# Optimization experiments

Measured on AMD Instinct MI355X. Metric: run time of the kernel, lower is better.

## Reference

```python
import jax, jax.numpy as jnp
import numpy as np

N_NODES = 100000


def gcn_conv(x, src, dst, deg_inv_sqrt, W, b):
    # x: [N, Fin], src/dst: [E_total] (self-loops included), W: [Fin, Fout]
    h = x @ W                                  # [N, Fout]
    norm = deg_inv_sqrt[src] * deg_inv_sqrt[dst]  # [E_total]
    msgs = h[src] * norm[:, None]              # [E_total, Fout] gather
    out = jax.ops.segment_sum(msgs, dst, num_segments=N_NODES)  # scatter-add
    return out + b


def setup_inputs() -> dict:
    key = jax.random.key(0)
    k1, k2, k3, k4, k5, k6, k7, k8 = jax.random.split(key, 8)
    input_dim, hidden_dim, out_dim = 4, 64, 2
    n_edges = 3200000
    x = jax.random.normal(k1, (N_NODES, input_dim), dtype=jnp.float32)
    edge_index = jax.random.randint(k2, (2, n_edges), 0, N_NODES, dtype=jnp.int64)
    s1 = 1.0 / np.sqrt(input_dim)
    s2 = 1.0 / np.sqrt(hidden_dim)
    W1 = jax.random.uniform(k3, (input_dim, hidden_dim), jnp.float32, -s1, s1)
    b1 = jnp.zeros((hidden_dim,), jnp.float32)
    W2 = jax.random.uniform(k4, (hidden_dim, hidden_dim), jnp.float32, -s2, s2)
    b2 = jnp.zeros((hidden_dim,), jnp.float32)
    Wf = jax.random.uniform(k5, (hidden_dim, out_dim), jnp.float32, -s2, s2)
    bf = jax.random.uniform(k6, (out_dim,), jnp.float32, -s2, s2)
    return {"x": x, "edge_index": edge_index, "W1": W1, "b1": b1,
            "W2": W2, "b2": b2, "Wf": Wf, "bf": bf}


def reference(x, edge_index, W1, b1, W2, b2, Wf, bf):
    # Add self-loops (PyG GCNConv default)
    loop = jnp.arange(N_NODES, dtype=edge_index.dtype)
    src = jnp.concatenate([edge_index[0], loop])
    dst = jnp.concatenate([edge_index[1], loop])
    # Symmetric normalization: degree on destination after self-loops
    deg = jax.ops.segment_sum(jnp.ones_like(dst, dtype=x.dtype), dst,
                              num_segments=N_NODES)
    deg_inv_sqrt = jnp.where(deg > 0, jax.lax.rsqrt(deg), 0.0)
    h = jax.nn.relu(gcn_conv(x, src, dst, deg_inv_sqrt, W1, b1))
    h = jax.nn.relu(gcn_conv(h, src, dst, deg_inv_sqrt, W2, b2))
    return h @ Wf + bf
```

## Files before the change

### kernel.cpp

```cpp
#include <hip/hip_runtime.h>
#include <hip/hip_bf16.h>

#define N_NODES 100000
#define N_EDGES 3200000
#define NB ((N_NODES + 255) / 256)
#define NBUCKET NB
#define EPB 8192
#define NPB ((N_EDGES + EPB - 1) / EPB)
#define BCAP 11264
#define KF_BLOCKS 1280
#define KF_WAVES (KF_BLOCKS * 4)

__device__ inline unsigned f2bf(float f) {
  unsigned x = __float_as_uint(f);
  return (x + 0x7FFFu + ((x >> 16) & 1u)) >> 16;
}


__global__ void __launch_bounds__(256) k_pass1(const int* __restrict__ src,
                                               const int* __restrict__ dst,
                                               int* __restrict__ gcur,
                                               unsigned int* __restrict__ eb) {
  __shared__ int hist[NBUCKET];
  __shared__ int gbase[NBUCKET];
  int tid = threadIdx.x;
  int base = blockIdx.x * EPB;
  int cnt = min(EPB, N_EDGES - base);
  int n4 = cnt >> 2;
  for (int i = tid; i < NBUCKET; i += 256) hist[i] = 0;
  __syncthreads();
  const int4* d4 = (const int4*)(dst + base);
  const int4* s4 = (const int4*)(src + base);
  unsigned mv[32];
  unsigned short mb[32];
#pragma unroll
  for (int k = 0; k < 8; ++k) {
    int i = tid + (k << 8);
    if (i < n4) {
      int4 dv = d4[i];
      int4 sv = s4[i];
      int b0 = dv.x >> 8, b1_ = dv.y >> 8, b2 = dv.z >> 8, b3 = dv.w >> 8;
      unsigned p0 = atomicAdd(&hist[b0], 1);
      unsigned p1 = atomicAdd(&hist[b1_], 1);
      unsigned p2 = atomicAdd(&hist[b2], 1);
      unsigned p3 = atomicAdd(&hist[b3], 1);
      mv[4 * k + 0] = (unsigned)sv.x | ((unsigned)(dv.x & 255) << 17) | (p0 << 25);
      mv[4 * k + 1] = (unsigned)sv.y | ((unsigned)(dv.y & 255) << 17) | (p1 << 25);
      mv[4 * k + 2] = (unsigned)sv.z | ((unsigned)(dv.z & 255) << 17) | (p2 << 25);
      mv[4 * k + 3] = (unsigned)sv.w | ((unsigned)(dv.w & 255) << 17) | (p3 << 25);
      mb[4 * k + 0] = (unsigned short)b0;
      mb[4 * k + 1] = (unsigned short)b1_;
      mb[4 * k + 2] = (unsigned short)b2;
      mb[4 * k + 3] = (unsigned short)b3;
    } else {
      mb[4 * k + 0] = 0xFFFF; mb[4 * k + 1] = 0xFFFF;
      mb[4 * k + 2] = 0xFFFF; mb[4 * k + 3] = 0xFFFF;
    }
  }
  __syncthreads();
  for (int b = tid; b < NBUCKET; b += 256) {
    int h = hist[b];
    gbase[b] = h ? atomicAdd(&gcur[b], h) : 0;
  }
  __syncthreads();
#pragma unroll
  for (int k = 0; k < 32; ++k) {
    if (mb[k] != 0xFFFF) {
      int b = mb[k];
      unsigned v = mv[k];
      unsigned pos = (unsigned)gbase[b] + (v >> 25);
      if (pos < BCAP) eb[(size_t)b * BCAP + pos] = v & 0x01FFFFFFu;
    }
  }
}


__global__ void __launch_bounds__(256) k_part2(unsigned int* __restrict__ eb,
                                               const int* __restrict__ gcur,
                                               int* __restrict__ rs, int* __restrict__ re,
                                               float* __restrict__ dis,
                                               const float4* __restrict__ x4,
                                               float4* __restrict__ xd) {
  __shared__ int hist[256], scn[256], cur[256];
  __shared__ int tot;
  __shared__ unsigned int stage[BCAP];
  int b = blockIdx.x, tid = threadIdx.x;
  int n0 = b << 8;
  int cnt = gcur[b];
  int base = b * BCAP;
  hist[tid] = 0; cur[tid] = 0;
  __syncthreads();
  for (int i = tid; i < cnt; i += 256)
    atomicAdd(&hist[eb[base + i] >> 17], 1);
  __syncthreads();
  int n = n0 + tid;
  int deg = hist[tid];
  int slots = (n < N_NODES) ? ((deg + 1 + 7) & ~7) : 0;
  int x = slots;
  scn[tid] = x;
  __syncthreads();
  for (int off = 1; off < 256; off <<= 1) {
    int t = (tid >= off) ? scn[tid - off] : 0;
    __syncthreads();
    x += t; scn[tid] = x;
    __syncthreads();
  }
  int excl = x - slots;
  if (tid == 255) tot = x;
  if (n < N_NODES) {
    rs[n]  = base + excl;
    re[n]  = base + excl + deg + 1;
    float dn = rsqrtf((float)(deg + 1));
    dis[n] = dn;
    float4 xv = x4[n];
    float4 w; w.x = xv.x * dn; w.y = xv.y * dn; w.z = xv.z * dn; w.w = xv.w * dn;
    xd[n] = w;
    stage[excl] = (unsigned)n;
    for (int i = deg + 1; i < slots; ++i)
      stage[excl + i] = (unsigned)N_NODES;
  }
  if (b == 0 && tid == 0) xd[N_NODES] = make_float4(0.f, 0.f, 0.f, 0.f);
  scn[tid] = excl + 1;
  __syncthreads();
  for (int i = tid; i < cnt; i += 256) {
    unsigned v = eb[base + i];
    unsigned low = v >> 17;
    int lpos = scn[low] + atomicAdd(&cur[low], 1);
    stage[lpos] = v & 0x1FFFFu;
  }
  __syncthreads();
  int total = tot;
  for (int i = tid; i < total; i += 256)
    eb[base + i] = stage[i];
  if (tid < 16) {
    int gp = total + tid;
    if (gp < BCAP) eb[base + gp] = (unsigned)N_NODES;
  }
}


__global__ void __launch_bounds__(256) k_l1(const float4* __restrict__ xd,
                                            const float* __restrict__ dis,
                                            const int* __restrict__ rs,
                                            const int* __restrict__ re,
                                            const int* __restrict__ csr,
                                            const float* __restrict__ W1,
                                            const float* __restrict__ b1,
                                            unsigned int* __restrict__ h1o) {
  int gt = blockIdx.x * 256 + threadIdx.x;
  int nid = gt >> 2, p = gt & 3;
  if (nid > N_NODES) return;
  if (nid == N_NODES) {
    uint4 z = make_uint4(0u, 0u, 0u, 0u);
    uint4* op = (uint4*)(h1o + nid * 32 + p * 8);
    op[0] = z; op[1] = z;
    return;
  }
  int e0 = rs[nid];
  int it4 = ((re[nid] - e0 + 7) & ~7) >> 2;
  const int* cp = csr + e0 + p;
  float ax = 0.f, ay = 0.f, az = 0.f, aw = 0.f;
#pragma unroll 4
  for (int t = 0; t < it4; ++t) {
    int s = cp[t << 2];
    float4 v = xd[s];
    ax += v.x; ay += v.y; az += v.z; aw += v.w;
  }
  ax += __shfl_xor(ax, 1); ax += __shfl_xor(ax, 2);
  ay += __shfl_xor(ay, 1); ay += __shfl_xor(ay, 2);
  az += __shfl_xor(az, 1); az += __shfl_xor(az, 2);
  aw += __shfl_xor(aw, 1); aw += __shfl_xor(aw, 2);
  float dn = dis[nid];
  ax *= dn; ay *= dn; az *= dn; aw *= dn;
  int j0 = p << 4;
  unsigned ou[8];
#pragma unroll
  for (int j2 = 0; j2 < 8; ++j2) {
    int j = j0 + j2 * 2;
    float s0 = b1[j]     + ax * W1[j]     + ay * W1[64 + j]     + az * W1[128 + j]     + aw * W1[192 + j];
    float s1 = b1[j + 1] + ax * W1[j + 1] + ay * W1[64 + j + 1] + az * W1[128 + j + 1] + aw * W1[192 + j + 1];
    unsigned u0 = f2bf(fmaxf(s0, 0.f) * dn);
    unsigned u1 = f2bf(fmaxf(s1, 0.f) * dn);
    ou[j2] = u0 | (u1 << 16);
  }
  uint4* op = (uint4*)(h1o + nid * 32 + p * 8);
  op[0] = make_uint4(ou[0], ou[1], ou[2], ou[3]);
  op[1] = make_uint4(ou[4], ou[5], ou[6], ou[7]);
}


__device__ inline void acc_bf2(float& a0, float& a1, unsigned u) {
  a0 += __uint_as_float(u << 16);
  a1 += __uint_as_float(u & 0xffff0000u);
}

__global__ void __launch_bounds__(256)
k_agg(const __hip_bfloat16* __restrict__ h1s, const float* __restrict__ dis,
      const int* __restrict__ rs, const int* __restrict__ re,
      const int* __restrict__ csr, float* __restrict__ agg) {
  int l = threadIdx.x & 63;
  int w = threadIdx.x >> 6;
  int n = blockIdx.x * 4 + w;
  int g = l >> 3;
  int c = l & 7;

  const unsigned int* h32 = (const unsigned int*)h1s;
  int e0 = rs[n];
  int iter = (re[n] - e0 + 7) >> 3;
  const int* cb = csr + e0 + g;
  int coff = c << 2;

  float a0 = 0.f, a1 = 0.f, a2 = 0.f, a3 = 0.f;
  float a4 = 0.f, a5 = 0.f, a6 = 0.f, a7 = 0.f;

  int s0 = cb[0];
  int s1 = (iter > 1) ? cb[8] : N_NODES;
  uint4 u0 = *(const uint4*)(h32 + (s0 << 5) + coff);
  uint4 u1 = *(const uint4*)(h32 + (s1 << 5) + coff);
  int sc2 = cb[16];
#pragma unroll 2
  for (int it = 0; it < iter; ++it) {
    int ss = (it + 2 < iter) ? sc2 : N_NODES;
    uint4 r = *(const uint4*)(h32 + (ss << 5) + coff);
    sc2 = cb[(it + 3) << 3];
    acc_bf2(a0, a1, u0.x); acc_bf2(a2, a3, u0.y);
    acc_bf2(a4, a5, u0.z); acc_bf2(a6, a7, u0.w);
    u0 = u1; u1 = r;
  }

#define RED3(a) a += __shfl_xor(a, 8); a += __shfl_xor(a, 16); a += __shfl_xor(a, 32);
  RED3(a0) RED3(a1) RED3(a2) RED3(a3) RED3(a4) RED3(a5) RED3(a6) RED3(a7)
#undef RED3

  float dn = dis[n];
  if (l < 8) {
    float4 v0; v0.x = a0 * dn; v0.y = a1 * dn; v0.z = a2 * dn; v0.w = a3 * dn;
    float4 v1; v1.x = a4 * dn; v1.y = a5 * dn; v1.z = a6 * dn; v1.w = a7 * dn;
    float4* ap = (float4*)(agg + (size_t)n * 64 + (l << 3));
    ap[0] = v0; ap[1] = v1;
  }
}


__global__ void __launch_bounds__(256)
k_final(const float* __restrict__ agg, const float* __restrict__ W2,
        const float* __restrict__ b2, const float* __restrict__ Wf,
        const float* __restrict__ bf, float* __restrict__ out) {
  int l = threadIdx.x & 63;
  int w = threadIdx.x >> 6;
  int wv = blockIdx.x * 4 + w;

  float wcol[64];
#pragma unroll
  for (int j = 0; j < 64; ++j) wcol[j] = W2[j * 64 + l];
  float bias = b2[l];
  float wf0 = Wf[l * 2 + 0];
  float wf1 = Wf[l * 2 + 1];
  float bf0 = bf[0], bf1 = bf[1];

  int n = wv;
  float av = agg[(size_t)n * 64 + l];
  while (true) {
    int n2 = n + KF_WAVES;
    float anext = 0.f;
    if (n2 < N_NODES) anext = agg[(size_t)n2 * 64 + l];

    unsigned ub = __float_as_uint(av);
    float t0 = bias, t1 = 0.f, t2 = 0.f, t3 = 0.f;
#pragma unroll
    for (int j = 0; j < 64; j += 4) {
      t0 = fmaf(__uint_as_float(__builtin_amdgcn_readlane(ub, j + 0)), wcol[j + 0], t0);
      t1 = fmaf(__uint_as_float(__builtin_amdgcn_readlane(ub, j + 1)), wcol[j + 1], t1);
      t2 = fmaf(__uint_as_float(__builtin_amdgcn_readlane(ub, j + 2)), wcol[j + 2], t2);
      t3 = fmaf(__uint_as_float(__builtin_amdgcn_readlane(ub, j + 3)), wcol[j + 3], t3);
    }
    float t = fmaxf((t0 + t1) + (t2 + t3), 0.f);

    float p0 = t * wf0;
    float p1 = t * wf1;
    for (int off = 32; off; off >>= 1) {
      p0 += __shfl_down(p0, off);
      p1 += __shfl_down(p1, off);
    }
    if (l == 0) {
      out[n * 2 + 0] = p0 + bf0;
      out[n * 2 + 1] = p1 + bf1;
    }
    if (n2 >= N_NODES) break;
    av = anext; n = n2;
  }
}


extern "C" void kernel_launch(void* const* d_in, const int* in_sizes, int n_in,
                              void* d_out, int out_size, void* d_ws, size_t ws_size,
                              hipStream_t stream) {
  const float* x  = (const float*)d_in[0];
  const int*   ei = (const int*)d_in[1];
  const float* W1 = (const float*)d_in[2];
  const float* b1 = (const float*)d_in[3];
  const float* W2 = (const float*)d_in[4];
  const float* b2 = (const float*)d_in[5];
  const float* Wf = (const float*)d_in[6];
  const float* bf = (const float*)d_in[7];
  float* out = (float*)d_out;

  const int* srcv = ei;
  const int* dstv = ei + N_EDGES;

  char* p = (char*)d_ws;
  auto take = [&](size_t bytes) { char* r = p; p += (bytes + 255) & ~(size_t)255; return r; };
  int*          gcur = (int*)take((size_t)NBUCKET * 4);
  unsigned int* eb   = (unsigned int*)take((size_t)NBUCKET * BCAP * 4 + 512);
  int*          rs   = (int*)take((size_t)N_NODES * 4);
  int*          re   = (int*)take((size_t)N_NODES * 4);
  float*        dis  = (float*)take((size_t)N_NODES * 4);
  float4*       xd   = (float4*)take((size_t)(N_NODES + 1) * 16);
  __hip_bfloat16* h1s = (__hip_bfloat16*)take((size_t)(N_NODES + 1) * 64 * 2);
  float*        agg  = (float*)take((size_t)N_NODES * 64 * 4);

  (void)hipMemsetAsync(gcur, 0, (size_t)NBUCKET * 4, stream);
  k_pass1<<<NPB, 256, 0, stream>>>(srcv, dstv, gcur, eb);
  k_part2<<<NBUCKET, 256, 0, stream>>>(eb, gcur, rs, re, dis, (const float4*)x, xd);
  const int* csr = (const int*)eb;
  k_l1<<<((N_NODES + 1) * 4 + 255) / 256, 256, 0, stream>>>(xd, dis, rs, re, csr, W1, b1, (unsigned int*)h1s);
  k_agg<<<N_NODES / 4, 256, 0, stream>>>(h1s, dis, rs, re, csr, agg);
  k_final<<<KF_BLOCKS, 256, 0, stream>>>(agg, W2, b2, Wf, bf, out);
}
```

Baseline: 239.2 us.

## Split bf16 hidden features into four column planes and aggregate per plane

The layer-1 output is stored as four separate 16-column bf16 planes instead of one 64-column row per node. The aggregation kernel launches one block group per plane, so each plane's gather working set (about 3.2 MB) can stay cache-resident. Each wave now processes four nodes serially, with 32 edges per iteration at two lanes per edge. Nontemporal loads and stores are added on the CSR, the degree arrays and the agg buffer to keep them from evicting the gathered features. The cost is that the CSR indices are read four times and there are more shuffle reductions per node.

```diff
diff --git a/kernel.cpp b/kernel.cpp
--- a/kernel.cpp
+++ b/kernel.cpp
@@ -2,6 +2,7 @@
 #include <hip/hip_bf16.h>
 
 #define N_NODES 100000
+#define NP1 (N_NODES + 1)
 #define N_EDGES 3200000
 #define NB ((N_NODES + 255) / 256)
 #define NBUCKET NB
@@ -10,6 +11,10 @@
 #define BCAP 11264
 #define KF_BLOCKS 1280
 #define KF_WAVES (KF_BLOCKS * 4)
+#define PBLK 6250
+
+typedef unsigned int uint4v __attribute__((ext_vector_type(4)));
+typedef float float4v __attribute__((ext_vector_type(4)));
 
 __device__ inline unsigned f2bf(float f) {
   unsigned x = __float_as_uint(f);
@@ -150,10 +155,11 @@
   int gt = blockIdx.x * 256 + threadIdx.x;
   int nid = gt >> 2, p = gt & 3;
   if (nid > N_NODES) return;
+  unsigned int* op32 = h1o + ((size_t)p * NP1 + nid) * 8;
   if (nid == N_NODES) {
-    uint4 z = make_uint4(0u, 0u, 0u, 0u);
-    uint4* op = (uint4*)(h1o + nid * 32 + p * 8);
-    op[0] = z; op[1] = z;
+    uint4v z = (uint4v)(0u);
+    __builtin_nontemporal_store(z, (uint4v*)op32);
+    __builtin_nontemporal_store(z, (uint4v*)op32 + 1);
     return;
   }
   int e0 = rs[nid];
@@ -162,7 +168,7 @@
   float ax = 0.f, ay = 0.f, az = 0.f, aw = 0.f;
 #pragma unroll 4
   for (int t = 0; t < it4; ++t) {
-    int s = cp[t << 2];
+    int s = __builtin_nontemporal_load(cp + (t << 2));
     float4 v = xd[s];
     ax += v.x; ay += v.y; az += v.z; aw += v.w;
   }
@@ -183,9 +189,10 @@
     unsigned u1 = f2bf(fmaxf(s1, 0.f) * dn);
     ou[j2] = u0 | (u1 << 16);
   }
-  uint4* op = (uint4*)(h1o + nid * 32 + p * 8);
-  op[0] = make_uint4(ou[0], ou[1], ou[2], ou[3]);
-  op[1] = make_uint4(ou[4], ou[5], ou[6], ou[7]);
+  uint4v o0; o0.x = ou[0]; o0.y = ou[1]; o0.z = ou[2]; o0.w = ou[3];
+  uint4v o1; o1.x = ou[4]; o1.y = ou[5]; o1.z = ou[6]; o1.w = ou[7];
+  __builtin_nontemporal_store(o0, (uint4v*)op32);
+  __builtin_nontemporal_store(o1, (uint4v*)op32 + 1);
 }
 
 
@@ -195,49 +202,60 @@
 }
 
 __global__ void __launch_bounds__(256)
-k_agg(const __hip_bfloat16* __restrict__ h1s, const float* __restrict__ dis,
+k_agg(const unsigned int* __restrict__ h1q,
+      const float* __restrict__ dis,
       const int* __restrict__ rs, const int* __restrict__ re,
       const int* __restrict__ csr, float* __restrict__ agg) {
   int l = threadIdx.x & 63;
   int w = threadIdx.x >> 6;
-  int n = blockIdx.x * 4 + w;
-  int g = l >> 3;
-  int c = l & 7;
-
-  const unsigned int* h32 = (const unsigned int*)h1s;
-  int e0 = rs[n];
-  int iter = (re[n] - e0 + 7) >> 3;
-  const int* cb = csr + e0 + g;
-  int coff = c << 2;
-
-  float a0 = 0.f, a1 = 0.f, a2 = 0.f, a3 = 0.f;
-  float a4 = 0.f, a5 = 0.f, a6 = 0.f, a7 = 0.f;
-
-  int s0 = cb[0];
-  int s1 = (iter > 1) ? cb[8] : N_NODES;
-  uint4 u0 = *(const uint4*)(h32 + (s0 << 5) + coff);
-  uint4 u1 = *(const uint4*)(h32 + (s1 << 5) + coff);
-  int sc2 = cb[16];
-#pragma unroll 2
-  for (int it = 0; it < iter; ++it) {
-    int ss = (it + 2 < iter) ? sc2 : N_NODES;
-    uint4 r = *(const uint4*)(h32 + (ss << 5) + coff);
-    sc2 = cb[(it + 3) << 3];
-    acc_bf2(a0, a1, u0.x); acc_bf2(a2, a3, u0.y);
-    acc_bf2(a4, a5, u0.z); acc_bf2(a6, a7, u0.w);
-    u0 = u1; u1 = r;
-  }
-
-#define RED3(a) a += __shfl_xor(a, 8); a += __shfl_xor(a, 16); a += __shfl_xor(a, 32);
-  RED3(a0) RED3(a1) RED3(a2) RED3(a3) RED3(a4) RED3(a5) RED3(a6) RED3(a7)
-#undef RED3
-
-  float dn = dis[n];
-  if (l < 8) {
-    float4 v0; v0.x = a0 * dn; v0.y = a1 * dn; v0.z = a2 * dn; v0.w = a3 * dn;
-    float4 v1; v1.x = a4 * dn; v1.y = a5 * dn; v1.z = a6 * dn; v1.w = a7 * dn;
-    float4* ap = (float4*)(agg + (size_t)n * 64 + (l << 3));
-    ap[0] = v0; ap[1] = v1;
+  int bid = blockIdx.x;
+  int plane = bid / PBLK;
+  int nb = bid - plane * PBLK;
+  int g = l >> 1;
+  int coff = (l & 1) << 2;
+  const unsigned int* pb = h1q + (size_t)plane * NP1 * 8;
+  int n0 = (nb * 4 + w) * 4;
+
+#pragma unroll 1
+  for (int j = 0; j < 4; ++j) {
+    int n = n0 + j;
+    int e0 = __builtin_nontemporal_load(rs + n);
+    int rlen = __builtin_nontemporal_load(re + n) - e0;
+    int slots = (rlen + 7) & ~7;
+    int iter = (slots + 31) >> 5;
+    const int* cb = csr + e0;
+
+    float a0 = 0.f, a1 = 0.f, a2 = 0.f, a3 = 0.f;
+    float a4 = 0.f, a5 = 0.f, a6 = 0.f, a7 = 0.f;
+
+    int s = __builtin_nontemporal_load(cb + g);
+    if (g >= slots) s = N_NODES;
+    uint4v u = *(const uint4v*)(pb + (s << 3) + coff);
+    for (int it = 1; it < iter; ++it) {
+      int off = g + (it << 5);
+      int s2 = __builtin_nontemporal_load(cb + off);
+      if (off >= slots) s2 = N_NODES;
+      uint4v r = *(const uint4v*)(pb + (s2 << 3) + coff);
+      acc_bf2(a0, a1, u.x); acc_bf2(a2, a3, u.y);
+      acc_bf2(a4, a5, u.z); acc_bf2(a6, a7, u.w);
+      u = r;
+    }
+    acc_bf2(a0, a1, u.x); acc_bf2(a2, a3, u.y);
+    acc_bf2(a4, a5, u.z); acc_bf2(a6, a7, u.w);
+
+#define RED5(a) a += __shfl_xor(a, 2); a += __shfl_xor(a, 4); a += __shfl_xor(a, 8); \
+                a += __shfl_xor(a, 16); a += __shfl_xor(a, 32);
+    RED5(a0) RED5(a1) RED5(a2) RED5(a3) RED5(a4) RED5(a5) RED5(a6) RED5(a7)
+#undef RED5
+
+    float dn = __builtin_nontemporal_load(dis + n);
+    if (l < 2) {
+      float4v v0; v0.x = a0 * dn; v0.y = a1 * dn; v0.z = a2 * dn; v0.w = a3 * dn;
+      float4v v1; v1.x = a4 * dn; v1.y = a5 * dn; v1.z = a6 * dn; v1.w = a7 * dn;
+      float4v* ap = (float4v*)(agg + (size_t)n * 64 + plane * 16 + (l << 3));
+      __builtin_nontemporal_store(v0, ap);
+      __builtin_nontemporal_store(v1, ap + 1);
+    }
   }
 }
 
@@ -259,11 +277,11 @@
   float bf0 = bf[0], bf1 = bf[1];
 
   int n = wv;
-  float av = agg[(size_t)n * 64 + l];
+  float av = __builtin_nontemporal_load(agg + (size_t)n * 64 + l);
   while (true) {
     int n2 = n + KF_WAVES;
     float anext = 0.f;
-    if (n2 < N_NODES) anext = agg[(size_t)n2 * 64 + l];
+    if (n2 < N_NODES) anext = __builtin_nontemporal_load(agg + (size_t)n2 * 64 + l);
 
     unsigned ub = __float_as_uint(av);
     float t0 = bias, t1 = 0.f, t2 = 0.f, t3 = 0.f;
@@ -316,14 +334,14 @@
   int*          re   = (int*)take((size_t)N_NODES * 4);
   float*        dis  = (float*)take((size_t)N_NODES * 4);
   float4*       xd   = (float4*)take((size_t)(N_NODES + 1) * 16);
-  __hip_bfloat16* h1s = (__hip_bfloat16*)take((size_t)(N_NODES + 1) * 64 * 2);
+  unsigned int* h1q  = (unsigned int*)take((size_t)4 * NP1 * 8 * 4);
   float*        agg  = (float*)take((size_t)N_NODES * 64 * 4);
 
   (void)hipMemsetAsync(gcur, 0, (size_t)NBUCKET * 4, stream);
   k_pass1<<<NPB, 256, 0, stream>>>(srcv, dstv, gcur, eb);
   k_part2<<<NBUCKET, 256, 0, stream>>>(eb, gcur, rs, re, dis, (const float4*)x, xd);
   const int* csr = (const int*)eb;
-  k_l1<<<((N_NODES + 1) * 4 + 255) / 256, 256, 0, stream>>>(xd, dis, rs, re, csr, W1, b1, (unsigned int*)h1s);
-  k_agg<<<N_NODES / 4, 256, 0, stream>>>(h1s, dis, rs, re, csr, agg);
+  k_l1<<<((N_NODES + 1) * 4 + 255) / 256, 256, 0, stream>>>(xd, dis, rs, re, csr, W1, b1, h1q);
+  k_agg<<<4 * PBLK, 256, 0, stream>>>(h1q, dis, rs, re, csr, agg);
   k_final<<<KF_BLOCKS, 256, 0, stream>>>(agg, W2, b2, Wf, bf, out);
 }
```

Measured after the change: 370.9 us. 55.0% more time.
